# Optimization experiments

Hardware: AMD Instinct MI355X
Metric: run time of the kernel (lower is better)

## Reference

```python
import jax, jax.numpy as jnp
import numpy as np


def setup_inputs() -> dict:
    key = jax.random.key(0)
    k1, k2, k3, k4 = jax.random.split(key, 4)
    B, T, C = 4, 1024, 768
    H, D = 12, 64
    scale = 0.02  # typical init scale for stability
    return {
        "x": jax.random.normal(k1, (B, T, C), dtype=jnp.float32),
        "Wq": jax.random.normal(k2, (H, C, D), dtype=jnp.float32) * scale,
        "Wk": jax.random.normal(k3, (H, C, D), dtype=jnp.float32) * scale,
        "Wv": jax.random.normal(k4, (H, C, D), dtype=jnp.float32) * scale,
    }


def reference(x, Wq, Wk, Wv):
    # x: [B,T,C]; Wq/Wk/Wv: [H,C,D]
    B, T, C = x.shape
    H, _, D = Wq.shape
    q = jnp.einsum("btc,hcd->bhtd", x, Wq)
    k = jnp.einsum("btc,hcd->bhtd", x, Wk)
    v = jnp.einsum("btc,hcd->bhtd", x, Wv)
    scores = jnp.einsum("bhtd,bhsd->bhts", q, k) * (D ** -0.5)
    causal = jnp.tril(jnp.ones((T, T), dtype=bool))
    scores = jnp.where(causal, scores, jnp.finfo(scores.dtype).min)
    attn = jax.nn.softmax(scores, axis=-1)
    out = jnp.einsum("bhts,bhsd->bhtd", attn, v)  # [B,H,T,D]
    # concat heads along last dim: [B,T,H*D]
    return out.transpose(0, 2, 1, 3).reshape(B, T, H * D)
```

## Files before the change

### kernel.cpp

```cpp
#include <hip/hip_runtime.h>
#include <math.h>
#include <stdint.h>

constexpr int B_ = 4, T_ = 1024, C_ = 768, H_ = 12, D_ = 64;
constexpr int BH_ = B_ * H_;
constexpr int M_ = B_ * T_;
constexpr int N_ = 3 * H_ * D_;

using f32x4 = __attribute__((ext_vector_type(4))) float;
using s16x8 = __attribute__((ext_vector_type(8))) short;

__device__ __forceinline__ unsigned short f2bf(float f) {
    union { float f; uint32_t u; } v; v.f = f;
    uint32_t u = v.u + 0x7fffu + ((v.u >> 16) & 1u);
    return (unsigned short)(u >> 16);
}

__global__ __launch_bounds__(256) void cast_x_kernel(
    const float* __restrict__ x, unsigned short* __restrict__ X16)
{
    int i = blockIdx.x * 256 + threadIdx.x;
    float4 v = ((const float4*)x)[i];
    ushort4 o;
    o.x = f2bf(v.x); o.y = f2bf(v.y); o.z = f2bf(v.z); o.w = f2bf(v.w);
    ((ushort4*)X16)[i] = o;
}

__global__ __launch_bounds__(256) void cast_w_kernel(
    const float* __restrict__ Wq, const float* __restrict__ Wk,
    const float* __restrict__ Wv, unsigned short* __restrict__ Wt)
{
    __shared__ unsigned short L[64][72];
    const int hp = blockIdx.x / 12, ct = blockIdx.x % 12;
    const int p = hp / H_, h = hp % H_;
    const float* W = (p == 0 ? Wq : (p == 1 ? Wk : Wv)) + (size_t)h * C_ * D_ + (size_t)ct * 64 * D_;
    const int tid = threadIdx.x;
#pragma unroll
    for (int it = 0; it < 4; ++it) {
        int f = tid + it * 256;
        int c = f >> 4, dg = f & 15;
        float4 v = ((const float4*)(W + (size_t)c * D_))[dg];
        L[dg * 4 + 0][c] = f2bf(v.x);
        L[dg * 4 + 1][c] = f2bf(v.y);
        L[dg * 4 + 2][c] = f2bf(v.z);
        L[dg * 4 + 3][c] = f2bf(v.w);
    }
    __syncthreads();
#pragma unroll
    for (int it = 0; it < 2; ++it) {
        int f = tid + it * 256;
        int d = f >> 3, cg = f & 7;
        uint4 v = *(const uint4*)&L[d][cg * 8];
        *(uint4*)(Wt + (size_t)(hp * 64 + d) * C_ + ct * 64 + cg * 8) = v;
    }
}

__global__ __launch_bounds__(256) void proj_kernel(
    const unsigned short* __restrict__ X16,
    const unsigned short* __restrict__ Wt,
    unsigned short* __restrict__ Qp,
    unsigned short* __restrict__ Kp,
    unsigned short* __restrict__ Vt)
{
    __shared__ unsigned short As[128 * 32];
    __shared__ unsigned short Bs[128 * 32];
    const int tid = threadIdx.x;
    const int l = tid & 63, w = tid >> 6;
    const int n0 = blockIdx.x * 128, m0 = blockIdx.y * 128;
    const int msub = (w >> 1) * 64, nsub = (w & 1) * 64;
    const int lr = l & 15, lg = l >> 4;

    f32x4 acc[4][4];
#pragma unroll
    for (int i = 0; i < 4; ++i)
#pragma unroll
        for (int j = 0; j < 4; ++j)
            acc[i][j] = (f32x4){0.f, 0.f, 0.f, 0.f};

    for (int k0 = 0; k0 < C_; k0 += 32) {
#pragma unroll
        for (int it = 0; it < 2; ++it) {
            int f = tid + it * 256;
            int m = f >> 2, kc = f & 3;
            uint4 va = *(const uint4*)(X16 + (size_t)(m0 + m) * C_ + k0 + kc * 8);
            *(uint4*)(As + f * 8) = va;
            uint4 vb = *(const uint4*)(Wt + (size_t)(n0 + m) * C_ + k0 + kc * 8);
            *(uint4*)(Bs + f * 8) = vb;
        }
        __syncthreads();
        s16x8 a[4], b[4];
#pragma unroll
        for (int i = 0; i < 4; ++i) {
            a[i] = *(const s16x8*)(As + (msub + i * 16 + lr) * 32 + lg * 8);
            b[i] = *(const s16x8*)(Bs + (nsub + i * 16 + lr) * 32 + lg * 8);
        }
#pragma unroll
        for (int i = 0; i < 4; ++i)
#pragma unroll
            for (int j = 0; j < 4; ++j)
                acc[i][j] = __builtin_amdgcn_mfma_f32_16x16x32_bf16(a[i], b[j], acc[i][j], 0, 0, 0);
        __syncthreads();
    }

    const int bq = m0 >> 10;
#pragma unroll
    for (int j = 0; j < 4; ++j) {
        int n = n0 + nsub + j * 16 + lr;
        int hp = n >> 6, d = n & 63;
        int p = hp / H_, hh = hp % H_;
        int bh = bq * H_ + hh;
#pragma unroll
        for (int i = 0; i < 4; ++i) {
            int tb = m0 + msub + i * 16 + lg * 4;
            int t = tb & (T_ - 1);
            if (p == 2) {
                ushort4 pv;
                pv.x = f2bf(acc[i][j][0]); pv.y = f2bf(acc[i][j][1]);
                pv.z = f2bf(acc[i][j][2]); pv.w = f2bf(acc[i][j][3]);
                *(ushort4*)(Vt + ((size_t)bh * D_ + d) * T_ + t) = pv;
            } else {
                unsigned short* P = (p == 0 ? Qp : Kp) + (size_t)bh * T_ * D_ + d;
#pragma unroll
                for (int r = 0; r < 4; ++r)
                    P[(size_t)(t + r) * D_] = f2bf(acc[i][j][r]);
            }
        }
    }
}

__global__ __launch_bounds__(64, 3) void attn_kernel(
    const unsigned short* __restrict__ Qp,
    const unsigned short* __restrict__ Kp,
    const unsigned short* __restrict__ Vt,
    float* __restrict__ out)
{
    __shared__ unsigned short Pl[16 * 72];
    const int l = threadIdx.x;
    const int lr = l & 15, lg = l >> 4;
    const int id = blockIdx.x;
    const int xcd = id & 7, rest = id >> 3;
    const int qi = rest & 63;
    const int bh = xcd + 8 * (rest >> 6);
    const int bq = bh / H_, hh = bh % H_;
    const unsigned short* Q = Qp + (size_t)bh * T_ * D_;
    const unsigned short* K = Kp + (size_t)bh * T_ * D_;
    const unsigned short* V = Vt + (size_t)bh * D_ * T_;
    float* O = out + (size_t)bq * T_ * (H_ * D_) + hh * D_;

    const float NEG = -30000.0f;
    const int q0 = qi * 16;

    s16x8 qa0 = *(const s16x8*)(Q + (size_t)(q0 + lr) * D_ + lg * 8);
    s16x8 qa1 = *(const s16x8*)(Q + (size_t)(q0 + lr) * D_ + 32 + lg * 8);

    f32x4 o[4];
    float m[4], ll[4];
#pragma unroll
    for (int g = 0; g < 4; ++g) o[g] = (f32x4){0.f, 0.f, 0.f, 0.f};
#pragma unroll
    for (int r = 0; r < 4; ++r) { m[r] = NEG; ll[r] = 0.f; }

    const int ntile = (qi >> 2) + 1;
    for (int j = 0; j < ntile; ++j) {
        const int kv0 = j * 64;
        s16x8 kb[8], vb[8];
#pragma unroll
        for (int g = 0; g < 4; ++g) {
            const unsigned short* kr = K + (size_t)(kv0 + g * 16 + lr) * D_ + lg * 8;
            kb[2 * g]     = *(const s16x8*)(kr);
            kb[2 * g + 1] = *(const s16x8*)(kr + 32);
        }
#pragma unroll
        for (int g = 0; g < 4; ++g) {
            const unsigned short* vr = V + (size_t)(g * 16 + lr) * T_ + kv0 + lg * 8;
            vb[2 * g]     = *(const s16x8*)(vr);
            vb[2 * g + 1] = *(const s16x8*)(vr + 32);
        }
        f32x4 s[4];
#pragma unroll
        for (int g = 0; g < 4; ++g) s[g] = (f32x4){0.f, 0.f, 0.f, 0.f};
#pragma unroll
        for (int g = 0; g < 4; ++g) {
            s[g] = __builtin_amdgcn_mfma_f32_16x16x32_bf16(qa0, kb[2 * g],     s[g], 0, 0, 0);
            s[g] = __builtin_amdgcn_mfma_f32_16x16x32_bf16(qa1, kb[2 * g + 1], s[g], 0, 0, 0);
        }
        const bool last = (j == ntile - 1);
        const float sc = 0.125f;
#pragma unroll
        for (int g = 0; g < 4; ++g)
#pragma unroll
            for (int r = 0; r < 4; ++r) {
                float v = s[g][r] * sc;
                if (last && (kv0 + g * 16 + lr > q0 + lg * 4 + r)) v = NEG;
                s[g][r] = v;
            }
#pragma unroll
        for (int r = 0; r < 4; ++r) {
            float mx = fmaxf(fmaxf(s[0][r], s[1][r]), fmaxf(s[2][r], s[3][r]));
            mx = fmaxf(mx, __shfl_xor(mx, 1));
            mx = fmaxf(mx, __shfl_xor(mx, 2));
            mx = fmaxf(mx, __shfl_xor(mx, 4));
            mx = fmaxf(mx, __shfl_xor(mx, 8));
            float mn = fmaxf(m[r], mx);
            float corr = __expf(m[r] - mn);
            float p[4], rs = 0.f;
#pragma unroll
            for (int g = 0; g < 4; ++g) { p[g] = __expf(s[g][r] - mn); rs += p[g]; }
            rs += __shfl_xor(rs, 1); rs += __shfl_xor(rs, 2);
            rs += __shfl_xor(rs, 4); rs += __shfl_xor(rs, 8);
            ll[r] = ll[r] * corr + rs;
            m[r] = mn;
#pragma unroll
            for (int g = 0; g < 4; ++g) {
                o[g][r] *= corr;
                Pl[(lg * 4 + r) * 72 + g * 16 + lr] = f2bf(p[g]);
            }
        }
        __syncthreads();

        s16x8 pa0 = *(const s16x8*)(Pl + lr * 72 + lg * 8);
        s16x8 pa1 = *(const s16x8*)(Pl + lr * 72 + 32 + lg * 8);
#pragma unroll
        for (int g = 0; g < 4; ++g) {
            o[g] = __builtin_amdgcn_mfma_f32_16x16x32_bf16(pa0, vb[2 * g],     o[g], 0, 0, 0);
            o[g] = __builtin_amdgcn_mfma_f32_16x16x32_bf16(pa1, vb[2 * g + 1], o[g], 0, 0, 0);
        }
        __syncthreads();
    }

    float rinv[4];
#pragma unroll
    for (int r = 0; r < 4; ++r) rinv[r] = 1.0f / ll[r];
#pragma unroll
    for (int g = 0; g < 4; ++g)
#pragma unroll
        for (int r = 0; r < 4; ++r)
            O[(size_t)(q0 + lg * 4 + r) * (H_ * D_) + g * 16 + lr] = o[g][r] * rinv[r];
}

extern "C" void kernel_launch(void* const* d_in, const int* in_sizes, int n_in,
                              void* d_out, int out_size, void* d_ws, size_t ws_size,
                              hipStream_t stream) {
    const float* x  = (const float*)d_in[0];
    const float* Wq = (const float*)d_in[1];
    const float* Wk = (const float*)d_in[2];
    const float* Wv = (const float*)d_in[3];
    float* out = (float*)d_out;

    char* ws = (char*)d_ws;
    unsigned short* X16 = (unsigned short*)(ws);
    unsigned short* Wt  = (unsigned short*)(ws + 6291456);
    unsigned short* Qp  = (unsigned short*)(ws + 9830400);
    unsigned short* Kp  = (unsigned short*)(ws + 16121856);
    unsigned short* Vt  = (unsigned short*)(ws + 22413312);

    cast_x_kernel<<<(M_ * C_ / 4) / 256, 256, 0, stream>>>(x, X16);
    cast_w_kernel<<<36 * 12, 256, 0, stream>>>(Wq, Wk, Wv, Wt);
    proj_kernel<<<dim3(N_ / 128, M_ / 128), 256, 0, stream>>>(X16, Wt, Qp, Kp, Vt);
    attn_kernel<<<BH_ * 64, 64, 0, stream>>>(Qp, Kp, Vt, out);
}
```

Measured before the change: 182.7 us.

## Transpose attention MFMA operands so each lane owns one query row

Measured after the change: 181.2 us. About the same (-0.8%).

```diff
diff --git a/kernel.cpp b/kernel.cpp
--- a/kernel.cpp
+++ b/kernel.cpp
@@ -134,7 +134,7 @@
     const unsigned short* __restrict__ Vt,
     float* __restrict__ out)
 {
-    __shared__ unsigned short Pl[16 * 72];
+    __shared__ unsigned short Pl[2][16 * 72];
     const int l = threadIdx.x;
     const int lr = l & 15, lg = l >> 4;
     const int id = blockIdx.x;
@@ -154,11 +154,9 @@
     s16x8 qa1 = *(const s16x8*)(Q + (size_t)(q0 + lr) * D_ + 32 + lg * 8);
 
     f32x4 o[4];
-    float m[4], ll[4];
 #pragma unroll
     for (int g = 0; g < 4; ++g) o[g] = (f32x4){0.f, 0.f, 0.f, 0.f};
-#pragma unroll
-    for (int r = 0; r < 4; ++r) { m[r] = NEG; ll[r] = 0.f; }
+    float m = NEG, ll = 0.f;
 
     const int ntile = (qi >> 2) + 1;
     for (int j = 0; j < ntile; ++j) {
@@ -179,11 +177,13 @@
         f32x4 s[4];
 #pragma unroll
         for (int g = 0; g < 4; ++g) s[g] = (f32x4){0.f, 0.f, 0.f, 0.f};
-#pragma unroll
-        for (int g = 0; g < 4; ++g) {
-            s[g] = __builtin_amdgcn_mfma_f32_16x16x32_bf16(qa0, kb[2 * g],     s[g], 0, 0, 0);
-            s[g] = __builtin_amdgcn_mfma_f32_16x16x32_bf16(qa1, kb[2 * g + 1], s[g], 0, 0, 0);
-        }
+        __builtin_amdgcn_s_setprio(1);
+#pragma unroll
+        for (int g = 0; g < 4; ++g) {
+            s[g] = __builtin_amdgcn_mfma_f32_16x16x32_bf16(kb[2 * g],     qa0, s[g], 0, 0, 0);
+            s[g] = __builtin_amdgcn_mfma_f32_16x16x32_bf16(kb[2 * g + 1], qa1, s[g], 0, 0, 0);
+        }
+        __builtin_amdgcn_s_setprio(0);
         const bool last = (j == ntile - 1);
         const float sc = 0.125f;
 #pragma unroll
@@ -191,51 +191,60 @@
 #pragma unroll
             for (int r = 0; r < 4; ++r) {
                 float v = s[g][r] * sc;
-                if (last && (kv0 + g * 16 + lr > q0 + lg * 4 + r)) v = NEG;
+                if (last && (kv0 + g * 16 + lg * 4 + r > q0 + lr)) v = NEG;
                 s[g][r] = v;
             }
-#pragma unroll
-        for (int r = 0; r < 4; ++r) {
-            float mx = fmaxf(fmaxf(s[0][r], s[1][r]), fmaxf(s[2][r], s[3][r]));
-            mx = fmaxf(mx, __shfl_xor(mx, 1));
-            mx = fmaxf(mx, __shfl_xor(mx, 2));
-            mx = fmaxf(mx, __shfl_xor(mx, 4));
-            mx = fmaxf(mx, __shfl_xor(mx, 8));
-            float mn = fmaxf(m[r], mx);
-            float corr = __expf(m[r] - mn);
-            float p[4], rs = 0.f;
-#pragma unroll
-            for (int g = 0; g < 4; ++g) { p[g] = __expf(s[g][r] - mn); rs += p[g]; }
-            rs += __shfl_xor(rs, 1); rs += __shfl_xor(rs, 2);
-            rs += __shfl_xor(rs, 4); rs += __shfl_xor(rs, 8);
-            ll[r] = ll[r] * corr + rs;
-            m[r] = mn;
-#pragma unroll
-            for (int g = 0; g < 4; ++g) {
+        float m0 = fmaxf(fmaxf(s[0][0], s[0][1]), fmaxf(s[0][2], s[0][3]));
+        float m1 = fmaxf(fmaxf(s[1][0], s[1][1]), fmaxf(s[1][2], s[1][3]));
+        float m2 = fmaxf(fmaxf(s[2][0], s[2][1]), fmaxf(s[2][2], s[2][3]));
+        float m3 = fmaxf(fmaxf(s[3][0], s[3][1]), fmaxf(s[3][2], s[3][3]));
+        float mx = fmaxf(fmaxf(m0, m1), fmaxf(m2, m3));
+        mx = fmaxf(mx, __shfl_xor(mx, 16));
+        mx = fmaxf(mx, __shfl_xor(mx, 32));
+        float mn = fmaxf(m, mx);
+        float corr = __expf(m - mn);
+        float rs = 0.f;
+#pragma unroll
+        for (int g = 0; g < 4; ++g)
+#pragma unroll
+            for (int r = 0; r < 4; ++r) {
+                s[g][r] = __expf(s[g][r] - mn);
+                rs += s[g][r];
+            }
+        rs += __shfl_xor(rs, 16);
+        rs += __shfl_xor(rs, 32);
+        ll = ll * corr + rs;
+        m = mn;
+#pragma unroll
+        for (int g = 0; g < 4; ++g)
+#pragma unroll
+            for (int r = 0; r < 4; ++r)
                 o[g][r] *= corr;
-                Pl[(lg * 4 + r) * 72 + g * 16 + lr] = f2bf(p[g]);
-            }
-        }
+        unsigned short* pb = Pl[j & 1];
+#pragma unroll
+        for (int g = 0; g < 4; ++g)
+#pragma unroll
+            for (int r = 0; r < 4; ++r)
+                pb[lr * 72 + g * 16 + lg * 4 + r] = f2bf(s[g][r]);
         __syncthreads();
-
-        s16x8 pa0 = *(const s16x8*)(Pl + lr * 72 + lg * 8);
-        s16x8 pa1 = *(const s16x8*)(Pl + lr * 72 + 32 + lg * 8);
-#pragma unroll
-        for (int g = 0; g < 4; ++g) {
-            o[g] = __builtin_amdgcn_mfma_f32_16x16x32_bf16(pa0, vb[2 * g],     o[g], 0, 0, 0);
-            o[g] = __builtin_amdgcn_mfma_f32_16x16x32_bf16(pa1, vb[2 * g + 1], o[g], 0, 0, 0);
-        }
-        __syncthreads();
-    }
-
-    float rinv[4];
-#pragma unroll
-    for (int r = 0; r < 4; ++r) rinv[r] = 1.0f / ll[r];
-#pragma unroll
-    for (int g = 0; g < 4; ++g)
-#pragma unroll
-        for (int r = 0; r < 4; ++r)
-            O[(size_t)(q0 + lg * 4 + r) * (H_ * D_) + g * 16 + lr] = o[g][r] * rinv[r];
+        s16x8 pa0 = *(const s16x8*)(pb + lr * 72 + lg * 8);
+        s16x8 pa1 = *(const s16x8*)(pb + lr * 72 + 32 + lg * 8);
+        __builtin_amdgcn_s_setprio(1);
+#pragma unroll
+        for (int g = 0; g < 4; ++g) {
+            o[g] = __builtin_amdgcn_mfma_f32_16x16x32_bf16(vb[2 * g],     pa0, o[g], 0, 0, 0);
+            o[g] = __builtin_amdgcn_mfma_f32_16x16x32_bf16(vb[2 * g + 1], pa1, o[g], 0, 0, 0);
+        }
+        __builtin_amdgcn_s_setprio(0);
+    }
+
+    const float rinv = 1.0f / ll;
+#pragma unroll
+    for (int g = 0; g < 4; ++g) {
+        float4 v = make_float4(o[g][0] * rinv, o[g][1] * rinv,
+                               o[g][2] * rinv, o[g][3] * rinv);
+        *(float4*)(O + (size_t)(q0 + lr) * (H_ * D_) + g * 16 + lg * 4) = v;
+    }
 }
 
 extern "C" void kernel_launch(void* const* d_in, const int* in_sizes, int n_in,
```
